# Kernel optimization log

Hardware: AMD Instinct MI355X
Metric: run time of the kernel (lower is better)

Reference implementation:

```python
import jax, jax.numpy as jnp
import numpy as np

B, D = 1024, 512   # batch, feature dim (input_shape[1])
K, NC = 256, 1     # output_dim, num_centers (mask broadcast requires NC==1)


def setup_inputs() -> dict:
    key = jax.random.key(0)
    k1, k2, k3 = jax.random.split(key, 3)
    x = jax.random.normal(k1, (B, D), dtype=jnp.float32)
    # w_mean params (keras Constant init in the original; randomized for a nontrivial test)
    means = jax.random.normal(k2, (K, NC, D), dtype=jnp.float32) * 0.1
    # w_rho params (keras 'uniform' init: U[-0.05, 0.05]); sigma = softplus(rho)
    rho = jax.random.uniform(k3, (K, NC, D), minval=-0.05, maxval=0.05, dtype=jnp.float32)
    return {"x": x, "means": means, "rho": rho}


def reference(x, means, rho):
    # sigma = log(1 + exp(rho)), computed in build()
    sigma = jnp.log1p(jnp.exp(rho))                      # (K, NC, D)
    # squared difference, broadcast over all classes/centers at once
    d2 = (x[None, None, :, :] - means[:, :, None, :]) ** 2   # (K, NC, B, D)
    sig2 = sigma * sigma                                  # (K, NC, D)
    # logits[idx*NC + c][b] = sum_d d2/2 * sigma^2
    logits = jnp.sum(d2 * (0.5 * sig2)[:, :, None, :], axis=-1)   # (K, NC, B)
    # gaussian activation: exp(-sum_d d2 / (2 sigma^2))
    G = jnp.exp(-jnp.sum(d2 / (2.0 * sig2)[:, :, None, :], axis=-1))  # (K, NC, B)
    # P = (max_c G * (NC+1) - sum_c G) / NC
    P = (jnp.max(G, axis=1) * (NC + 1) - jnp.sum(G, axis=1)) / NC     # (K, B)
    probs = P.T                                           # (B, K)
    # stack order in TF: idx-major, c-minor -> (B, K*NC)
    logits_bk = jnp.transpose(logits, (2, 0, 1))          # (B, K, NC)
    mask = (probs >= 0.0).astype(logits_bk.dtype)         # (B, K)
    out = logits_bk * mask[:, :, None]                    # broadcast over NC (==1)
    return out.reshape(B, K * NC)
```

## Files before the change

### kernel.cpp

```cpp
#include <hip/hip_runtime.h>
#include <hip/hip_bf16.h>


#define BB 1024
#define DD 512
#define DP 1024
#define KK 256
#define PREP_X_BLOCKS 512
#define PREP_W_BLOCKS 128

typedef __attribute__((ext_vector_type(8))) short bf16x8;
typedef __attribute__((ext_vector_type(4))) float f32x4;
typedef __attribute__((ext_vector_type(4))) unsigned short us4;

static __device__ inline unsigned short f2bf(float f) {
    __hip_bfloat16 h = __float2bfloat16(f);
    return *reinterpret_cast<unsigned short*>(&h);
}

__global__ __launch_bounds__(256) void prep_kernel(const float* __restrict__ x,
                                                   const float* __restrict__ means,
                                                   const float* __restrict__ rho,
                                                   unsigned short* __restrict__ Xp,
                                                   unsigned short* __restrict__ Wp,
                                                   float* __restrict__ c) {
    const int t = threadIdx.x;
    if (blockIdx.x < PREP_X_BLOCKS) {
        const int i = blockIdx.x * 256 + t;
        const int b  = i >> 7;
        const int d4 = (i & 127) * 4;
        const float4 xv = *(const float4*)&x[b * DD + d4];
        us4 sq, ln;
        sq.x = f2bf(xv.x * xv.x); sq.y = f2bf(xv.y * xv.y);
        sq.z = f2bf(xv.z * xv.z); sq.w = f2bf(xv.w * xv.w);
        ln.x = f2bf(xv.x); ln.y = f2bf(xv.y); ln.z = f2bf(xv.z); ln.w = f2bf(xv.w);
        *(us4*)&Xp[b * DP + d4]      = sq;
        *(us4*)&Xp[b * DP + DD + d4] = ln;
    } else {
        __shared__ float red[256];
        const int blk  = blockIdx.x - PREP_X_BLOCKS;
        const int half = t >> 7;
        const int k    = blk * 2 + half;
        const int d4   = (t & 127) * 4;
        const float4 mv = *(const float4*)&means[k * DD + d4];
        const float4 rv = *(const float4*)&rho  [k * DD + d4];
        us4 wq, aq;
        float sp, wv, csum = 0.f;
        sp = log1pf(expf(rv.x)); wv = 0.5f * sp * sp;
        wq.x = f2bf(wv); aq.x = f2bf(-2.f * wv * mv.x); csum += wv * mv.x * mv.x;
        sp = log1pf(expf(rv.y)); wv = 0.5f * sp * sp;
        wq.y = f2bf(wv); aq.y = f2bf(-2.f * wv * mv.y); csum += wv * mv.y * mv.y;
        sp = log1pf(expf(rv.z)); wv = 0.5f * sp * sp;
        wq.z = f2bf(wv); aq.z = f2bf(-2.f * wv * mv.z); csum += wv * mv.z * mv.z;
        sp = log1pf(expf(rv.w)); wv = 0.5f * sp * sp;
        wq.w = f2bf(wv); aq.w = f2bf(-2.f * wv * mv.w); csum += wv * mv.w * mv.w;
        *(us4*)&Wp[k * DD * 2 / 1 + d4] = wq;
        *(us4*)&Wp[k * DP + DD + d4] = aq;
        red[t] = csum;
        __syncthreads();
        if (t < 2) {
            float s = 0.f;
#pragma unroll
            for (int j = 0; j < 128; j++) s += red[t * 128 + j];
            c[blk * 2 + t] = s;
        }
    }
}

__global__ __launch_bounds__(256) void gemm_kernel(const unsigned short* __restrict__ Xp,
                                                   const unsigned short* __restrict__ Wp,
                                                   const float* __restrict__ c,
                                                   float* __restrict__ out) {
    const int lane = threadIdx.x & 63;
    const int wave = threadIdx.x >> 6;
    const int tile = blockIdx.x * 4 + wave;
    const int kb = tile & 15;
    const int bb = tile >> 4;
    const int k0 = kb * 16;
    const int b0 = bb * 16;

    const int rc   = lane & 15;
    const int quad = lane >> 4;

    const unsigned short* aRow = Xp + (b0 + rc) * DP + quad * 8;
    const unsigned short* bRow = Wp + (k0 + rc) * DP + quad * 8;

    f32x4 acc = {0.f, 0.f, 0.f, 0.f};
#pragma unroll 8
    for (int dk = 0; dk < DP; dk += 32) {
        const bf16x8 a = *(const bf16x8*)(aRow + dk);
        const bf16x8 b = *(const bf16x8*)(bRow + dk);
        acc = __builtin_amdgcn_mfma_f32_16x16x32_bf16(a, b, acc, 0, 0, 0);
    }

    const float cv = c[k0 + rc];
#pragma unroll
    for (int r = 0; r < 4; r++) {
        out[(b0 + quad * 4 + r) * KK + (k0 + rc)] = acc[r] + cv;
    }
}

extern "C" void kernel_launch(void* const* d_in, const int* in_sizes, int n_in,
                              void* d_out, int out_size, void* d_ws, size_t ws_size,
                              hipStream_t stream) {
    const float* x     = (const float*)d_in[0];
    const float* means = (const float*)d_in[1];
    const float* rho   = (const float*)d_in[2];
    float* out = (float*)d_out;

    unsigned short* Xp = (unsigned short*)d_ws;
    unsigned short* Wp = Xp + (size_t)BB * DP;
    float* c = (float*)(Wp + (size_t)KK * DP);

    prep_kernel<<<PREP_X_BLOCKS + PREP_W_BLOCKS, 256, 0, stream>>>(x, means, rho, Xp, Wp, c);
    gemm_kernel<<<256, 256, 0, stream>>>(Xp, Wp, c, out);
}
```

Baseline: 68.62 us.

## Fuse prep and GEMM into one kernel with on-the-fly weight transform

Merges the preprocessing and bf16 MFMA GEMM kernels into a single launch. Each block converts its 16 rows of x into a swizzled LDS tile, and each wave computes the softplus weights, the mean-scaled terms and the constant term directly from means and rho in registers before issuing its MFMAs. This removes a kernel launch and the workspace round trip through global memory. In exchange, the transcendental work on the weights is repeated across the 64 batch-row blocks, and it now uses the fast __logf/__expf intrinsics.

```diff
diff --git a/kernel.cpp b/kernel.cpp
--- a/kernel.cpp
+++ b/kernel.cpp
@@ -4,10 +4,7 @@
 
 #define BB 1024
 #define DD 512
-#define DP 1024
 #define KK 256
-#define PREP_X_BLOCKS 512
-#define PREP_W_BLOCKS 128
 
 typedef __attribute__((ext_vector_type(8))) short bf16x8;
 typedef __attribute__((ext_vector_type(4))) float f32x4;
@@ -18,85 +15,82 @@
     return *reinterpret_cast<unsigned short*>(&h);
 }
 
-__global__ __launch_bounds__(256) void prep_kernel(const float* __restrict__ x,
-                                                   const float* __restrict__ means,
-                                                   const float* __restrict__ rho,
-                                                   unsigned short* __restrict__ Xp,
-                                                   unsigned short* __restrict__ Wp,
-                                                   float* __restrict__ c) {
-    const int t = threadIdx.x;
-    if (blockIdx.x < PREP_X_BLOCKS) {
-        const int i = blockIdx.x * 256 + t;
-        const int b  = i >> 7;
-        const int d4 = (i & 127) * 4;
-        const float4 xv = *(const float4*)&x[b * DD + d4];
-        us4 sq, ln;
-        sq.x = f2bf(xv.x * xv.x); sq.y = f2bf(xv.y * xv.y);
-        sq.z = f2bf(xv.z * xv.z); sq.w = f2bf(xv.w * xv.w);
-        ln.x = f2bf(xv.x); ln.y = f2bf(xv.y); ln.z = f2bf(xv.z); ln.w = f2bf(xv.w);
-        *(us4*)&Xp[b * DP + d4]      = sq;
-        *(us4*)&Xp[b * DP + DD + d4] = ln;
-    } else {
-        __shared__ float red[256];
-        const int blk  = blockIdx.x - PREP_X_BLOCKS;
-        const int half = t >> 7;
-        const int k    = blk * 2 + half;
-        const int d4   = (t & 127) * 4;
-        const float4 mv = *(const float4*)&means[k * DD + d4];
-        const float4 rv = *(const float4*)&rho  [k * DD + d4];
-        us4 wq, aq;
-        float sp, wv, csum = 0.f;
-        sp = log1pf(expf(rv.x)); wv = 0.5f * sp * sp;
-        wq.x = f2bf(wv); aq.x = f2bf(-2.f * wv * mv.x); csum += wv * mv.x * mv.x;
-        sp = log1pf(expf(rv.y)); wv = 0.5f * sp * sp;
-        wq.y = f2bf(wv); aq.y = f2bf(-2.f * wv * mv.y); csum += wv * mv.y * mv.y;
-        sp = log1pf(expf(rv.z)); wv = 0.5f * sp * sp;
-        wq.z = f2bf(wv); aq.z = f2bf(-2.f * wv * mv.z); csum += wv * mv.z * mv.z;
-        sp = log1pf(expf(rv.w)); wv = 0.5f * sp * sp;
-        wq.w = f2bf(wv); aq.w = f2bf(-2.f * wv * mv.w); csum += wv * mv.w * mv.w;
-        *(us4*)&Wp[k * DD * 2 / 1 + d4] = wq;
-        *(us4*)&Wp[k * DP + DD + d4] = aq;
-        red[t] = csum;
-        __syncthreads();
-        if (t < 2) {
-            float s = 0.f;
+static __device__ inline int swz(int r, int col) {
+    return r * 2048 + ((col * 2) ^ ((r & 7) << 4));
+}
+
+__global__ __launch_bounds__(256) void fused_kernel(const float* __restrict__ x,
+                                                    const float* __restrict__ means,
+                                                    const float* __restrict__ rho,
+                                                    float* __restrict__ out) {
+    __shared__ char Xs[32768];
+
+    const int t  = threadIdx.x;
+    const int bb = blockIdx.x >> 2;
+    const int b0 = bb * 16;
+
+    {
+        const int r = t >> 4;
+        const int l = t & 15;
+        const float4* xrow = (const float4*)(x + (size_t)(b0 + r) * DD);
 #pragma unroll
-            for (int j = 0; j < 128; j++) s += red[t * 128 + j];
-            c[blk * 2 + t] = s;
+        for (int i = 0; i < 8; i++) {
+            const float4 v = xrow[l + 16 * i];
+            const int c = (l + 16 * i) * 4;
+            us4 sq, ln;
+            sq.x = f2bf(v.x * v.x); sq.y = f2bf(v.y * v.y);
+            sq.z = f2bf(v.z * v.z); sq.w = f2bf(v.w * v.w);
+            ln.x = f2bf(v.x); ln.y = f2bf(v.y); ln.z = f2bf(v.z); ln.w = f2bf(v.w);
+            *(us4*)(Xs + swz(r, c))      = sq;
+            *(us4*)(Xs + swz(r, DD + c)) = ln;
         }
     }
-}
+    __syncthreads();
 
-__global__ __launch_bounds__(256) void gemm_kernel(const unsigned short* __restrict__ Xp,
-                                                   const unsigned short* __restrict__ Wp,
-                                                   const float* __restrict__ c,
-                                                   float* __restrict__ out) {
-    const int lane = threadIdx.x & 63;
-    const int wave = threadIdx.x >> 6;
-    const int tile = blockIdx.x * 4 + wave;
-    const int kb = tile & 15;
-    const int bb = tile >> 4;
-    const int k0 = kb * 16;
-    const int b0 = bb * 16;
-
+    const int lane = t & 63;
+    const int wave = t >> 6;
+    const int kb   = (blockIdx.x & 3) * 4 + wave;
+    const int k0   = kb * 16;
     const int rc   = lane & 15;
     const int quad = lane >> 4;
 
-    const unsigned short* aRow = Xp + (b0 + rc) * DP + quad * 8;
-    const unsigned short* bRow = Wp + (k0 + rc) * DP + quad * 8;
+    const float4* mBase = (const float4*)(means + (size_t)(k0 + rc) * DD) + quad * 2;
+    const float4* rBase = (const float4*)(rho   + (size_t)(k0 + rc) * DD) + quad * 2;
 
     f32x4 acc = {0.f, 0.f, 0.f, 0.f};
-#pragma unroll 8
-    for (int dk = 0; dk < DP; dk += 32) {
-        const bf16x8 a = *(const bf16x8*)(aRow + dk);
-        const bf16x8 b = *(const bf16x8*)(bRow + dk);
-        acc = __builtin_amdgcn_mfma_f32_16x16x32_bf16(a, b, acc, 0, 0, 0);
+    float csum = 0.f;
+
+#pragma unroll 4
+    for (int j = 0; j < 16; j++) {
+        const float4 m0 = mBase[8 * j];
+        const float4 m1 = mBase[8 * j + 1];
+        const float4 r0 = rBase[8 * j];
+        const float4 r1 = rBase[8 * j + 1];
+
+        const float mm[8] = {m0.x, m0.y, m0.z, m0.w, m1.x, m1.y, m1.z, m1.w};
+        const float rr[8] = {r0.x, r0.y, r0.z, r0.w, r1.x, r1.y, r1.z, r1.w};
+        bf16x8 wq, aq;
+#pragma unroll
+        for (int e = 0; e < 8; e++) {
+            const float sp = __logf(1.f + __expf(rr[e]));
+            const float wv = 0.5f * sp * sp;
+            wq[e] = (short)f2bf(wv);
+            aq[e] = (short)f2bf(-2.f * wv * mm[e]);
+            csum += wv * mm[e] * mm[e];
+        }
+
+        const bf16x8 a_sq = *(const bf16x8*)(Xs + swz(rc, quad * 8 + 32 * j));
+        const bf16x8 a_ln = *(const bf16x8*)(Xs + swz(rc, DD + quad * 8 + 32 * j));
+        acc = __builtin_amdgcn_mfma_f32_16x16x32_bf16(a_sq, wq, acc, 0, 0, 0);
+        acc = __builtin_amdgcn_mfma_f32_16x16x32_bf16(a_ln, aq, acc, 0, 0, 0);
     }
 
-    const float cv = c[k0 + rc];
+    csum += __shfl_xor(csum, 16);
+    csum += __shfl_xor(csum, 32);
+
 #pragma unroll
     for (int r = 0; r < 4; r++) {
-        out[(b0 + quad * 4 + r) * KK + (k0 + rc)] = acc[r] + cv;
+        out[(size_t)(b0 + quad * 4 + r) * KK + (k0 + rc)] = acc[r] + csum;
     }
 }
 
@@ -107,11 +101,7 @@
     const float* means = (const float*)d_in[1];
     const float* rho   = (const float*)d_in[2];
     float* out = (float*)d_out;
+    (void)d_ws; (void)ws_size;
 
-    unsigned short* Xp = (unsigned short*)d_ws;
-    unsigned short* Wp = Xp + (size_t)BB * DP;
-    float* c = (float*)(Wp + (size_t)KK * DP);
-
-    prep_kernel<<<PREP_X_BLOCKS + PREP_W_BLOCKS, 256, 0, stream>>>(x, means, rho, Xp, Wp, c);
-    gemm_kernel<<<256, 256, 0, stream>>>(Xp, Wp, c, out);
+    fused_kernel<<<256, 256, 0, stream>>>(x, means, rho, out);
 }
```

After: 69.09 us. Within noise of the previous version (+0.7%).
